# Performance work log

Hardware: AMD Instinct MI355X
Metric: run time of the kernel (lower is better)

Reference implementation:

```python
import jax, jax.numpy as jnp
import numpy as np

# Masked BatchNorm: per-channel stats over valid (masked) elements only.
def _masked_bn(x, mask, gamma, beta, eps=1e-5):
    m = mask.astype(x.dtype)  # (B,1,N[,K])
    axes = tuple([0] + list(range(2, x.ndim)))
    n = jnp.maximum(jnp.sum(m, axis=axes), 1.0)
    mean = jnp.sum(x * m, axis=axes) / n  # (C,)
    shp = (1, x.shape[1]) + (1,) * (x.ndim - 2)
    mu = mean.reshape(shp)
    var = jnp.sum(jnp.square(x - mu) * m, axis=axes) / n
    xn = (x - mu) * jax.lax.rsqrt(var.reshape(shp) + eps)
    return xn * gamma.reshape(shp) + beta.reshape(shp)

def _lrelu(x):
    return jnp.where(x >= 0, x, 0.2 * x)  # LeakyReLU(0.2)

MIN_NBR = 1  # config['neighbourhood']['min']

def _edge_block(x, idx, valid, W, g, b):
    # x: (B,C,N), idx: (B,N,K) neighbour indices, valid: (B,N,K) bool
    B, C, N = x.shape
    xt = jnp.transpose(x, (0, 2, 1))  # (B,N,C)
    nbr = xt[jnp.arange(B)[:, None, None], idx]  # (B,N,K,C) gather
    ctr = xt[:, :, None, :]
    f = jnp.concatenate([nbr - ctr, jnp.broadcast_to(ctr, nbr.shape)], axis=-1)  # (B,N,K,2C)
    f = f * valid[..., None].astype(f.dtype)
    f = jnp.transpose(f, (0, 3, 1, 2))  # (B,2C,N,K)
    h = jnp.einsum('oc,bcnk->bonk', W, f)  # 1x1 conv2d, no bias
    h = _lrelu(_masked_bn(h, valid[:, None, :, :], g, b))
    h = jnp.max(jnp.where(valid[:, None, :, :], h, -jnp.inf), axis=-1)  # masked max over K
    ok = jnp.sum(valid, axis=-1) >= MIN_NBR  # (B,N)
    h = jnp.where(ok[:, None, :], h, 0.0)
    return h, ok


def setup_inputs() -> dict:
    key = jax.random.key(0)
    ks = jax.random.split(key, 12)
    B, N, K = 8, 2048, 20
    f32 = jnp.float32
    def w(k, shape):
        return jax.random.normal(k, shape, f32) * 0.05
    d = {}
    d['x'] = jax.random.normal(ks[0], (B, 3, N), f32)
    d['idx'] = jax.random.randint(ks[1], (B, N, K), 0, N)
    d['valid'] = jax.random.randint(ks[2], (B, N, K), 0, 2).astype(bool)
    enc_dims = [(64, 6), (64, 128), (128, 128), (256, 256)]
    for i, (o, c) in enumerate(enc_dims, 1):
        d['enc_w%d' % i] = w(jax.random.fold_in(key, 10 + i), (o, c))
        d['enc_g%d' % i] = jnp.ones((o,), f32)
        d['enc_b%d' % i] = jnp.zeros((o,), f32)
    d['last_w'] = w(ks[3], (1024, 512)); d['last_g'] = jnp.ones((1024,), f32); d['last_b'] = jnp.zeros((1024,), f32)
    d['emb_w1'] = w(ks[4], (512, 1024)); d['emb_bias1'] = jnp.zeros((512,), f32); d['emb_g1'] = jnp.ones((512,), f32); d['emb_b1'] = jnp.zeros((512,), f32)
    d['emb_w2'] = w(ks[5], (128, 512)); d['emb_bias2'] = jnp.zeros((128,), f32); d['emb_g2'] = jnp.ones((128,), f32); d['emb_b2'] = jnp.zeros((128,), f32)
    d['out_w'] = w(ks[6], (32, 128)); d['out_bias'] = jnp.zeros((32,), f32)
    return d


def reference(x, idx, valid, enc_w1, enc_g1, enc_b1, enc_w2, enc_g2, enc_b2, enc_w3, enc_g3, enc_b3, enc_w4, enc_g4, enc_b4, last_w, last_g, last_b, emb_w1, emb_bias1, emb_g1, emb_b1, emb_w2, emb_bias2, emb_g2, emb_b2, out_w, out_bias):
    inter = []
    ok_all = jnp.ones((x.shape[0], x.shape[2]), dtype=bool)
    for W, g, b in ((enc_w1, enc_g1, enc_b1), (enc_w2, enc_g2, enc_b2), (enc_w3, enc_g3, enc_b3), (enc_w4, enc_g4, enc_b4)):
        x, ok = _edge_block(x, idx, valid, W, g, b)
        inter.append(x)
        ok_all = jnp.logical_and(ok_all, ok)
    x = jnp.concatenate(inter, axis=1)  # (B,512,N)
    m = ok_all[:, None, :]
    x = _lrelu(_masked_bn(jnp.einsum('oc,bcn->bon', last_w, x), m, last_g, last_b))
    x = jnp.einsum('oc,bcn->bon', emb_w1, x) + emb_bias1[None, :, None]
    x = _lrelu(_masked_bn(x, m, emb_g1, emb_b1))
    x = jnp.einsum('oc,bcn->bon', emb_w2, x) + emb_bias2[None, :, None]
    x = _lrelu(_masked_bn(x, m, emb_g2, emb_b2))
    return jnp.einsum('oc,bcn->bon', out_w, x) + out_bias[None, :, None]  # (B,32,N)
```

## Files before the change

### kernel.cpp

```cpp
#include <hip/hip_runtime.h>
#include <hip/hip_bf16.h>
#include <cstdint>
#include <cstddef>

constexpr int B_  = 8;
constexpr int N_  = 2048;
constexpr int KNB = 20;
constexpr int MN  = B_ * N_;
constexpr int CAT_C = 512;
constexpr float EPS = 1e-5f;

typedef __attribute__((ext_vector_type(8))) short bf16x8;
typedef __attribute__((ext_vector_type(4))) float f32x4;

constexpr size_t alignup64(size_t x){ return (x + 63) & ~size_t(63); }
constexpr size_t STATS   = 0;
constexpr size_t NSTATS  = size_t(7) * 8 * 2048;
constexpr size_t MISC    = STATS + NSTATS;
constexpr size_t SCALEO  = alignup64(MISC + 16);
constexpr size_t SHIFTO  = SCALEO + 7 * 1024;
constexpr size_t CIDX    = alignup64(SHIFTO + 7 * 1024);
constexpr size_t OK8     = alignup64(CIDX + size_t(MN) * KNB);
constexpr size_t WENC    = alignup64(OK8 + (MN + 3) / 4);
constexpr size_t WLAST   = WENC  + 32768;
constexpr size_t WEMB1   = WLAST + 262144;
constexpr size_t WEMB2   = WEMB1 + 262144;
constexpr size_t XT      = WEMB2 + 32768;
constexpr size_t XCATB   = alignup64(XT + size_t(MN) * 4);
constexpr size_t HHOFF   = XCATB + size_t(MN) * 256;
constexpr size_t HMAXO   = HHOFF + size_t(MN) * 512;
constexpr size_t HMINO   = HMAXO + size_t(MN) * 256;
constexpr size_t YLB     = HMINO + size_t(MN) * 256;

__device__ inline float bf2f(unsigned short u){
    unsigned int x = ((unsigned int)u) << 16;
    return __builtin_bit_cast(float, x);
}
__device__ inline unsigned short f2bf(float f){
    __hip_bfloat16 h = __float2bfloat16(f);
    return __builtin_bit_cast(unsigned short, h);
}
__device__ inline unsigned int packbf(float a, float b){
    return (unsigned int)f2bf(a) | ((unsigned int)f2bf(b) << 16);
}
__device__ inline float lrelu(float v){ return fmaxf(v, 0.2f * v); }
__device__ inline void gl16(const void* g, void* l){
    __builtin_amdgcn_global_load_lds(
        (const __attribute__((address_space(1))) void*)g,
        (__attribute__((address_space(3))) void*)l, 16, 0, 0);
}


__global__ __launch_bounds__(256) void detect_valid_kernel(const unsigned char* __restrict__ v, int* __restrict__ flag){
    __shared__ int f;
    if (threadIdx.x == 0) f = 1;
    __syncthreads();
    int ok = 1;
    #pragma unroll
    for (int it = 0; it < 4; ++it){
        int g = threadIdx.x + it * 256;
        unsigned char b0 = v[4*g], b1 = v[4*g+1], b2 = v[4*g+2], b3 = v[4*g+3];
        if ((b1 | b2 | b3) != 0 || b0 > 1) ok = 0;
    }
    if (!ok) atomicAnd(&f, 0);
    __syncthreads();
    if (threadIdx.x == 0) *flag = f;
}

__global__ __launch_bounds__(256) void expand_ok_kernel(const void* __restrict__ vin,
        const int* __restrict__ idx, int* __restrict__ ci, unsigned char* __restrict__ ok,
        float* __restrict__ nvalid, float* __restrict__ n_ok, const int* __restrict__ flag){
    const int p = blockIdx.x * 256 + threadIdx.x;
    int jj[KNB];
    const int4* ip4 = (const int4*)(idx + (size_t)p * KNB);
    #pragma unroll
    for (int q = 0; q < 5; ++q){
        int4 iv = ip4[q];
        jj[q*4+0] = iv.x; jj[q*4+1] = iv.y; jj[q*4+2] = iv.z; jj[q*4+3] = iv.w;
    }
    bool val[KNB];
    if (*flag){
        const int* vi = ((const int*)vin) + (size_t)p * KNB;
        #pragma unroll
        for (int k = 0; k < KNB; ++k) val[k] = vi[k] != 0;
    } else {
        const unsigned char* vb = ((const unsigned char*)vin) + (size_t)p * KNB;
        #pragma unroll
        for (int k = 0; k < KNB; ++k) val[k] = vb[k] != 0;
    }
    int cnt = 0;
    int* dst = ci + (size_t)p * KNB;
    #pragma unroll
    for (int k = 0; k < KNB; ++k){
        if (val[k]) dst[cnt++] = jj[k];
    }
    ok[p] = (unsigned char)cnt;
    float fc = (float)cnt;
    #pragma unroll
    for (int o = 32; o > 0; o >>= 1) fc += __shfl_down(fc, o);
    unsigned long long m = __ballot(cnt != 0);
    if ((threadIdx.x & 63) == 0){
        if (fc > 0.f) unsafeAtomicAdd(nvalid, fc);
        if (m)        unsafeAtomicAdd(n_ok, (float)__popcll(m));
    }
}

__global__ __launch_bounds__(256) void transpose_x_kernel(const float* __restrict__ x, float* __restrict__ xt){
    int i = blockIdx.x * 256 + threadIdx.x;
    if (i >= MN) return;
    int b = i / N_, n = i % N_;
    float4 v;
    v.x = x[(size_t)(b*3 + 0) * N_ + n];
    v.y = x[(size_t)(b*3 + 1) * N_ + n];
    v.z = x[(size_t)(b*3 + 2) * N_ + n];
    v.w = 0.f;
    ((float4*)xt)[i] = v;
}

__global__ __launch_bounds__(256) void build_wcomb_f32_kernel(const float* __restrict__ W, float* __restrict__ wc,
        int O, int C){
    int i = blockIdx.x * 256 + threadIdx.x;
    if (i >= 2 * O * C) return;
    int r = i / C, c = i % C;
    float v;
    if (r < O) v = W[(size_t)r * (2*C) + c];
    else       v = W[(size_t)(r-O) * (2*C) + C + c] - W[(size_t)(r-O) * (2*C) + c];
    wc[i] = v;
}

__global__ __launch_bounds__(256) void build_wcomb_bf16_kernel(const float* __restrict__ W, unsigned short* __restrict__ wc,
        int O, int C){
    int i = blockIdx.x * 256 + threadIdx.x;
    if (i >= 2 * O * C) return;
    int r = i / C, c = i % C;
    float v;
    if (r < O) v = W[(size_t)r * (2*C) + c];
    else       v = W[(size_t)(r-O) * (2*C) + C + c] - W[(size_t)(r-O) * (2*C) + c];
    wc[i] = f2bf(v);
}

__global__ __launch_bounds__(256) void convert3_bf16_kernel(
        const float* __restrict__ a, const float* __restrict__ b, const float* __restrict__ c,
        unsigned short* __restrict__ wa, unsigned short* __restrict__ wb, unsigned short* __restrict__ wcc){
    int i = blockIdx.x * 256 + threadIdx.x;
    if (i >= 278528) return;
    const float* src; unsigned short* dst; int off;
    if (i < 131072)      { src = a; dst = wa;  off = i; }
    else if (i < 262144) { src = b; dst = wb;  off = i - 131072; }
    else                 { src = c; dst = wcc; off = i - 262144; }
    float4 v = ((const float4*)src)[off];
    ushort4 o;
    o.x = f2bf(v.x); o.y = f2bf(v.y); o.z = f2bf(v.z); o.w = f2bf(v.w);
    ((ushort4*)dst)[off] = o;
}

__global__ __launch_bounds__(256) void gemm_f32(
        const float* __restrict__ X, const float* __restrict__ W,
        float* __restrict__ Y, const float* __restrict__ bias,
        int M, int K, int O, int lda, int ldy,
        const float* __restrict__ scX, const float* __restrict__ shX)
{
    __shared__ float Xs[16][68];
    __shared__ float Ws[16][68];
    const int tid = threadIdx.x;
    const int tx = tid & 15, ty = tid >> 4;
    const int m0 = blockIdx.x * 64, o0 = blockIdx.y * 64;
    float acc[4][4] = {};
    for (int k0 = 0; k0 < K; k0 += 16){
        #pragma unroll
        for (int i = 0; i < 4; ++i){
            int e = tid + i * 256;
            int r = e >> 4, c = e & 15;
            float xv = 0.f, wv = 0.f;
            if (k0 + c < K){
                xv = X[(size_t)(m0 + r) * lda + k0 + c];
                if (scX){
                    xv = lrelu(xv * scX[k0 + c] + shX[k0 + c]);
                }
                if (o0 + r < O) wv = W[(size_t)(o0 + r) * K + k0 + c];
            }
            Xs[c][r] = xv;
            Ws[c][r] = wv;
        }
        __syncthreads();
        #pragma unroll
        for (int kk = 0; kk < 16; ++kk){
            const float4 a4 = *(const float4*)(&Xs[kk][ty * 4]);
            const float4 b4 = *(const float4*)(&Ws[kk][tx * 4]);
            const float a[4] = {a4.x, a4.y, a4.z, a4.w};
            const float b[4] = {b4.x, b4.y, b4.z, b4.w};
            #pragma unroll
            for (int i = 0; i < 4; ++i)
                #pragma unroll
                for (int j = 0; j < 4; ++j)
                    acc[i][j] = fmaf(a[i], b[j], acc[i][j]);
        }
        __syncthreads();
    }
    #pragma unroll
    for (int i = 0; i < 4; ++i){
        int m = m0 + ty * 4 + i;
        int o = o0 + tx * 4;
        if (o < O){
            float4 v;
            v.x = acc[i][0]; v.y = acc[i][1]; v.z = acc[i][2]; v.w = acc[i][3];
            if (bias){
                v.x += bias[o]; v.y += bias[o+1]; v.z += bias[o+2]; v.w += bias[o+3];
            }
            *(float4*)(&Y[(size_t)m * ldy + o]) = v;
        }
    }
}

template<bool OBF16, bool STATSF, bool AFFA>
__global__ __launch_bounds__(256) void gemm_bf16_mfma(
        const unsigned short* __restrict__ Xg, const unsigned short* __restrict__ Wg,
        void* __restrict__ Yv, const float* __restrict__ bias,
        int K, int ldx, int ldy,
        const unsigned char* __restrict__ ok, float* __restrict__ statsL,
        const float* __restrict__ scA, const float* __restrict__ shA)
{
    __shared__ unsigned short As[128 * 64];
    __shared__ unsigned short Bs[128 * 64];
    __shared__ float scsh[AFFA ? 2048 : 2];
    const int t = threadIdx.x;
    const int lane = t & 63;
    const int w = t >> 6;
    const int wr = w >> 1, wc = w & 1;
    const int m0 = blockIdx.x * 128;
    const int o0 = blockIdx.y * 128;

    if constexpr (AFFA){
        for (int v = t; v < K; v += 256){
            scsh[v] = scA[v];
            scsh[1024 + v] = shA[v];
        }
        __syncthreads();
    }

    f32x4 acc[4][4] = {};

    for (int k0 = 0; k0 < K; k0 += 64){
        #pragma unroll
        for (int i = 0; i < 4; ++i){
            int e = i * 256 + t;
            int row = e >> 3;
            int c = (e & 7) ^ (row & 7);
            int kk = k0 + c * 8;
            if constexpr (AFFA){
                uint4 a = *(const uint4*)(Xg + (size_t)(m0 + row) * ldx + kk);
                float4 s0 = *(const float4*)&scsh[kk], s1 = *(const float4*)&scsh[kk + 4];
                float4 h0 = *(const float4*)&scsh[1024 + kk], h1 = *(const float4*)&scsh[1024 + kk + 4];
                const float sc[8] = {s0.x,s0.y,s0.z,s0.w, s1.x,s1.y,s1.z,s1.w};
                const float sh[8] = {h0.x,h0.y,h0.z,h0.w, h1.x,h1.y,h1.z,h1.w};
                unsigned int wds[4] = {a.x, a.y, a.z, a.w};
                unsigned int ov[4];
                #pragma unroll
                for (int q = 0; q < 4; ++q){
                    float f0 = lrelu(bf2f((unsigned short)(wds[q] & 0xffffu)) * sc[2*q]   + sh[2*q]);
                    float f1 = lrelu(bf2f((unsigned short)(wds[q] >> 16))     * sc[2*q+1] + sh[2*q+1]);
                    ov[q] = packbf(f0, f1);
                }
                uint4 o4 = {ov[0], ov[1], ov[2], ov[3]};
                *(uint4*)&As[(size_t)e * 8] = o4;
            } else {
                gl16(Xg + (size_t)(m0 + row) * ldx + kk, &As[(size_t)e * 8]);
            }
            gl16(Wg + (size_t)(o0 + row) * K + kk, &Bs[(size_t)e * 8]);
        }
        __syncthreads();
        const int kq = lane >> 4;
        #pragma unroll
        for (int ks = 0; ks < 2; ++ks){
            bf16x8 a[4], b[4];
            #pragma unroll
            for (int mi = 0; mi < 4; ++mi){
                int r = wr * 64 + mi * 16 + (lane & 15);
                int ch = (ks * 4 + kq) ^ (r & 7);
                a[mi] = *(const bf16x8*)&As[r * 64 + ch * 8];
            }
            #pragma unroll
            for (int ni = 0; ni < 4; ++ni){
                int r = wc * 64 + ni * 16 + (lane & 15);
                int ch = (ks * 4 + kq) ^ (r & 7);
                b[ni] = *(const bf16x8*)&Bs[r * 64 + ch * 8];
            }
            #pragma unroll
            for (int mi = 0; mi < 4; ++mi)
                #pragma unroll
                for (int ni = 0; ni < 4; ++ni)
                    acc[mi][ni] = __builtin_amdgcn_mfma_f32_16x16x32_bf16(a[mi], b[ni], acc[mi][ni], 0, 0, 0);
        }
        __syncthreads();
    }

    float s1l[4] = {}, s2l[4] = {};
    float bi[4];
    #pragma unroll
    for (int ni = 0; ni < 4; ++ni)
        bi[ni] = bias ? bias[o0 + wc * 64 + ni * 16 + (lane & 15)] : 0.f;

    #pragma unroll
    for (int mi = 0; mi < 4; ++mi){
        const int mbase = m0 + wr * 64 + mi * 16 + (lane >> 4) * 4;
        uchar4 okv = {1,1,1,1};
        if constexpr (STATSF) okv = *(const uchar4*)(ok + mbase);
        const unsigned char okarr[4] = {okv.x, okv.y, okv.z, okv.w};
        #pragma unroll
        for (int j = 0; j < 4; ++j){
            const int m = mbase + j;
            #pragma unroll
            for (int ni = 0; ni < 4; ++ni){
                int o = o0 + wc * 64 + ni * 16 + (lane & 15);
                float v = acc[mi][ni][j] + bi[ni];
                if constexpr (STATSF){
                    if (okarr[j]){ s1l[ni] += v; s2l[ni] += v * v; }
                }
                if constexpr (OBF16)
                    ((unsigned short*)Yv)[(size_t)m * ldy + o] = f2bf(v);
                else
                    ((float*)Yv)[(size_t)m * ldy + o] = v;
            }
        }
    }

    if constexpr (STATSF){
        #pragma unroll
        for (int ni = 0; ni < 4; ++ni){
            s1l[ni] += __shfl_xor(s1l[ni], 16); s1l[ni] += __shfl_xor(s1l[ni], 32);
            s2l[ni] += __shfl_xor(s2l[ni], 16); s2l[ni] += __shfl_xor(s2l[ni], 32);
        }
        if ((lane >> 4) == 0){
            float* S = statsL + (size_t)((blockIdx.x + blockIdx.y) & 7) * 2048;
            #pragma unroll
            for (int ni = 0; ni < 4; ++ni){
                int o = o0 + wc * 64 + ni * 16 + lane;
                unsafeAtomicAdd(&S[o],        s1l[ni]);
                unsafeAtomicAdd(&S[1024 + o], s2l[ni]);
            }
        }
    }
}

template<int T>
__global__ __launch_bounds__(256) void edge_gather_kernel(
        const float* __restrict__ HHp, const int* __restrict__ ci,
        const unsigned char* __restrict__ okc, const float* __restrict__ g,
        float* __restrict__ hmaxo, float* __restrict__ hmino,
        float* __restrict__ statsL)
{
    constexpr int O = 64 * T, TWO2 = 2 * O;
    __shared__ float ls[4][2][64 * T];
    const int bid  = blockIdx.x;
    const int wv   = threadIdx.x >> 6;
    const int lane = threadIdx.x & 63;
    const int bat  = bid & 7;
    const int chunk = bid >> 3;
    const int base = bat << 11;
    const int p0   = base + chunk * 8 + wv * 2;

    bool ln = false;
    #pragma unroll
    for (int t = 0; t < T; ++t) if (g[lane + 64 * t] < 0.f) ln = true;
    const bool needmin = (__ballot(ln) != 0ull);

    float s1[T] = {}, s2[T] = {};
    #pragma unroll
    for (int pi = 0; pi < 2; ++pi){
        const int p = p0 + pi;
        const int cnt = okc[p];
        int jj[KNB];
        const int4* ip4 = (const int4*)(ci + (size_t)p * KNB);
        #pragma unroll
        for (int q = 0; q < 5; ++q){
            int4 iv = ip4[q];
            jj[q*4+0] = iv.x; jj[q*4+1] = iv.y; jj[q*4+2] = iv.z; jj[q*4+3] = iv.w;
        }
        float hc[T], hmax[T], hmin[T];
        #pragma unroll
        for (int t = 0; t < T; ++t){
            hc[t] = HHp[(size_t)p * TWO2 + O + lane + 64 * t];
            hmax[t] = -INFINITY; hmin[t] = INFINITY;
        }
        if (needmin){
            int k = 0;
            for (; k + 4 <= cnt; k += 4){
                #pragma unroll
                for (int u = 0; u < 4; ++u){
                    const float* row = HHp + (size_t)(base + jj[k + u]) * TWO2 + lane;
                    #pragma unroll
                    for (int t = 0; t < T; ++t){
                        float h = row[64 * t] + hc[t];
                        s1[t] += h; s2[t] += h * h;
                        hmax[t] = fmaxf(hmax[t], h);
                        hmin[t] = fminf(hmin[t], h);
                    }
                }
            }
            for (; k < cnt; ++k){
                const float* row = HHp + (size_t)(base + jj[k]) * TWO2 + lane;
                #pragma unroll
                for (int t = 0; t < T; ++t){
                    float h = row[64 * t] + hc[t];
                    s1[t] += h; s2[t] += h * h;
                    hmax[t] = fmaxf(hmax[t], h);
                    hmin[t] = fminf(hmin[t], h);
                }
            }
        } else {
            int k = 0;
            for (; k + 4 <= cnt; k += 4){
                #pragma unroll
                for (int u = 0; u < 4; ++u){
                    const float* row = HHp + (size_t)(base + jj[k + u]) * TWO2 + lane;
                    #pragma unroll
                    for (int t = 0; t < T; ++t){
                        float h = row[64 * t] + hc[t];
                        s1[t] += h; s2[t] += h * h;
                        hmax[t] = fmaxf(hmax[t], h);
                    }
                }
            }
            for (; k < cnt; ++k){
                const float* row = HHp + (size_t)(base + jj[k]) * TWO2 + lane;
                #pragma unroll
                for (int t = 0; t < T; ++t){
                    float h = row[64 * t] + hc[t];
                    s1[t] += h; s2[t] += h * h;
                    hmax[t] = fmaxf(hmax[t], h);
                }
            }
        }
        #pragma unroll
        for (int t = 0; t < T; ++t)
            __builtin_nontemporal_store(hmax[t], &hmaxo[(size_t)p * O + lane + 64 * t]);
        if (needmin){
            #pragma unroll
            for (int t = 0; t < T; ++t)
                __builtin_nontemporal_store(hmin[t], &hmino[(size_t)p * O + lane + 64 * t]);
        }
    }
    #pragma unroll
    for (int t = 0; t < T; ++t){
        ls[wv][0][64 * t + lane] = s1[t];
        ls[wv][1][64 * t + lane] = s2[t];
    }
    __syncthreads();
    float* S = statsL + (size_t)(bid & 7) * 2048;
    for (int v = threadIdx.x; v < 128 * T; v += 256){
        const int half = v / (64 * T);
        const int ch   = v - half * 64 * T;
        float s = ls[0][half][ch] + ls[1][half][ch] + ls[2][half][ch] + ls[3][half][ch];
        unsafeAtomicAdd(&S[half * 1024 + ch], s);
    }
}

__global__ void bn_params_kernel(const float* __restrict__ statsL, const float* __restrict__ cnt,
        const float* __restrict__ g, const float* __restrict__ bta,
        float* __restrict__ scale, float* __restrict__ shift, int O)
{
    int o = blockIdx.x * 256 + threadIdx.x;
    if (o >= O) return;
    float s1 = 0.f, s2 = 0.f;
    #pragma unroll
    for (int r = 0; r < 8; ++r){
        s1 += statsL[(size_t)r * 2048 + o];
        s2 += statsL[(size_t)r * 2048 + 1024 + o];
    }
    float n   = fmaxf(*cnt, 1.0f);
    float mu  = s1 / n;
    float var = fmaxf(s2 / n - mu * mu, 0.f);
    float sc  = g[o] * rsqrtf(var + EPS);
    scale[o] = sc;
    shift[o] = bta[o] - mu * sc;
}

__global__ __launch_bounds__(256) void edge_finalize_kernel(
        const float* __restrict__ hmaxo, const float* __restrict__ hmino,
        const unsigned char* __restrict__ ok,
        const float* __restrict__ scale, const float* __restrict__ shift,
        unsigned short* __restrict__ xcat, int O, int chanoff)
{
    size_t i = (size_t)blockIdx.x * 256 + threadIdx.x;
    size_t p = i / (size_t)O;
    int o = (int)(i - p * (size_t)O);
    float v = 0.f;
    if (ok[p]){
        float sc = scale[o];
        float h;
        if (sc >= 0.f) h = hmaxo[i]; else h = hmino[i];
        v = lrelu(h * sc + shift[o]);
    }
    xcat[p * CAT_C + chanoff + o] = f2bf(v);
}

__global__ __launch_bounds__(256) void transpose_out_kernel(const float* __restrict__ Y, float* __restrict__ out){
    int i = blockIdx.x * 256 + threadIdx.x;
    int n = i & (N_ - 1);
    int rest = i >> 11;
    int o = rest & 31;
    int b = rest >> 5;
    out[i] = Y[((((size_t)b * N_) + n) << 5) + o];
}

extern "C" void kernel_launch(void* const* d_in, const int* in_sizes, int n_in,
                              void* d_out, int out_size, void* d_ws, size_t ws_size,
                              hipStream_t stream)
{
    const float* x        = (const float*)d_in[0];
    const int*   idx      = (const int*)  d_in[1];
    const void*  valid_rw = d_in[2];
    const float* enc_w[4] = {(const float*)d_in[3], (const float*)d_in[6], (const float*)d_in[9],  (const float*)d_in[12]};
    const float* enc_g[4] = {(const float*)d_in[4], (const float*)d_in[7], (const float*)d_in[10], (const float*)d_in[13]};
    const float* enc_b[4] = {(const float*)d_in[5], (const float*)d_in[8], (const float*)d_in[11], (const float*)d_in[14]};
    const float* last_w   = (const float*)d_in[15];
    const float* last_g   = (const float*)d_in[16];
    const float* last_b   = (const float*)d_in[17];
    const float* emb_w1   = (const float*)d_in[18];
    const float* emb_bi1  = (const float*)d_in[19];
    const float* emb_g1   = (const float*)d_in[20];
    const float* emb_b1   = (const float*)d_in[21];
    const float* emb_w2   = (const float*)d_in[22];
    const float* emb_bi2  = (const float*)d_in[23];
    const float* emb_g2   = (const float*)d_in[24];
    const float* emb_b2   = (const float*)d_in[25];
    const float* out_w    = (const float*)d_in[26];
    const float* out_bias = (const float*)d_in[27];

    float* ws = (float*)d_ws;
    int*   ci   = (int*)(ws + CIDX);
    unsigned char* ok8  = (unsigned char*)(ws + OK8);
    unsigned short* xcatb = (unsigned short*)(ws + XCATB);
    unsigned short* ylb   = (unsigned short*)(ws + YLB);
    unsigned short* wlastb = (unsigned short*)(ws + WLAST);
    unsigned short* wemb1b = (unsigned short*)(ws + WEMB1);
    unsigned short* wemb2b = (unsigned short*)(ws + WEMB2);
    float* nvalid = ws + MISC + 0;
    float* n_ok   = ws + MISC + 1;
    int*   flag   = (int*)(ws + MISC + 2);

    hipMemsetAsync(d_ws, 0, (MISC + 16) * sizeof(float), stream);

    detect_valid_kernel<<<1, 256, 0, stream>>>((const unsigned char*)valid_rw, flag);
    expand_ok_kernel<<<MN / 256, 256, 0, stream>>>(valid_rw, idx, ci, ok8, nvalid, n_ok, flag);
    transpose_x_kernel<<<MN / 256, 256, 0, stream>>>(x, ws + XT);
    convert3_bf16_kernel<<<(278528 + 255) / 256, 256, 0, stream>>>(last_w, emb_w1, emb_w2, wlastb, wemb1b, wemb2b);

    const int Cs[4]     = {3, 64, 64, 128};
    const int Os[4]     = {64, 64, 128, 256};
    const int inoff[4]  = {0, 0, 64, 128};
    const int outoff[4] = {0, 64, 128, 256};

    for (int L = 0; L < 4; ++L){
        const int C = Cs[L], O = Os[L], TWO2 = 2 * O;
        if (L == 0){
            build_wcomb_f32_kernel<<<(2*O*C + 255)/256, 256, 0, stream>>>(enc_w[L], ws + WENC, O, C);
            dim3 gg(MN / 64, TWO2 / 64);
            gemm_f32<<<gg, 256, 0, stream>>>(ws + XT, ws + WENC, ws + HHOFF, nullptr, MN, C, TWO2, 4, TWO2, nullptr, nullptr);
        } else {
            build_wcomb_bf16_kernel<<<(2*O*C + 255)/256, 256, 0, stream>>>(enc_w[L], (unsigned short*)(ws + WENC), O, C);
            dim3 gg(MN / 128, TWO2 / 128);
            gemm_bf16_mfma<false, false, false><<<gg, 256, 0, stream>>>(xcatb + inoff[L], (unsigned short*)(ws + WENC),
                    ws + HHOFF, nullptr, C, CAT_C, TWO2, nullptr, nullptr, nullptr, nullptr);
        }
        float* statsL = ws + STATS + (size_t)L * 8 * 2048;
        const int gather_blocks = MN / 8;
        switch (O / 64){
            case 1: edge_gather_kernel<1><<<gather_blocks, 256, 0, stream>>>(ws + HHOFF, ci, ok8, enc_g[L], ws + HMAXO, ws + HMINO, statsL); break;
            case 2: edge_gather_kernel<2><<<gather_blocks, 256, 0, stream>>>(ws + HHOFF, ci, ok8, enc_g[L], ws + HMAXO, ws + HMINO, statsL); break;
            case 4: edge_gather_kernel<4><<<gather_blocks, 256, 0, stream>>>(ws + HHOFF, ci, ok8, enc_g[L], ws + HMAXO, ws + HMINO, statsL); break;
        }
        float* scl = ws + SCALEO + (size_t)L * 1024;
        float* shf = ws + SHIFTO + (size_t)L * 1024;
        bn_params_kernel<<<(O + 255)/256, 256, 0, stream>>>(statsL, nvalid, enc_g[L], enc_b[L], scl, shf, O);
        edge_finalize_kernel<<<(int)(((size_t)MN * O) / 256), 256, 0, stream>>>(
            ws + HMAXO, ws + HMINO, ok8, scl, shf, xcatb, O, outoff[L]);
    }

    unsigned short* yemb1b = (unsigned short*)(ws + HMAXO);
    float* yemb2 = ws + HMINO;
    float* yout  = ws + HHOFF;

    float* scl4 = ws + SCALEO + 4 * 1024, *shf4 = ws + SHIFTO + 4 * 1024;
    float* scl5 = ws + SCALEO + 5 * 1024, *shf5 = ws + SHIFTO + 5 * 1024;
    float* scl6 = ws + SCALEO + 6 * 1024, *shf6 = ws + SHIFTO + 6 * 1024;

    {
        float* statsL = ws + STATS + (size_t)4 * 8 * 2048;
        dim3 gg(MN / 128, 1024 / 128);
        gemm_bf16_mfma<true, true, false><<<gg, 256, 0, stream>>>(xcatb, wlastb, ylb, nullptr, 512, CAT_C, 1024,
                ok8, statsL, nullptr, nullptr);
        bn_params_kernel<<<4, 256, 0, stream>>>(statsL, n_ok, last_g, last_b, scl4, shf4, 1024);
    }
    {
        float* statsL = ws + STATS + (size_t)5 * 8 * 2048;
        dim3 gg(MN / 128, 512 / 128);
        gemm_bf16_mfma<true, true, true><<<gg, 256, 0, stream>>>(ylb, wemb1b, yemb1b, emb_bi1, 1024, 1024, 512,
                ok8, statsL, scl4, shf4);
        bn_params_kernel<<<2, 256, 0, stream>>>(statsL, n_ok, emb_g1, emb_b1, scl5, shf5, 512);
    }
    {
        float* statsL = ws + STATS + (size_t)6 * 8 * 2048;
        dim3 gg(MN / 128, 128 / 128);
        gemm_bf16_mfma<false, true, true><<<gg, 256, 0, stream>>>(yemb1b, wemb2b, yemb2, emb_bi2, 512, 512, 128,
                ok8, statsL, scl5, shf5);
        bn_params_kernel<<<1, 256, 0, stream>>>(statsL, n_ok, emb_g2, emb_b2, scl6, shf6, 128);
    }
    {
        dim3 gg(MN / 64, 1);
        gemm_f32<<<gg, 256, 0, stream>>>(yemb2, out_w, yout, out_bias, MN, 128, 32, 128, 32, scl6, shf6);
        transpose_out_kernel<<<(B_ * 32 * N_) / 256, 256, 0, stream>>>(yout, (float*)d_out);
    }
}
```

Measured before the change: 387.3 us.

## Fold BN parameter computation into producer kernels and merge prep launches

Removes the separate bn_params kernels by having the last block of each stats-producing kernel (edge gather and fused GEMMs) compute scale and shift, chosen through an atomic completion counter and threadfence. Merges the valid-format detection into expand_ok, and merges the x transpose, weight bf16 conversions and all four edge-weight combinations into one prep kernel. This cuts roughly a dozen small kernel launches and their dependency gaps. In exchange, every block of those kernels now pays for a fence and a counter atomic, and each block of expand_ok repeats the detection scan.

```diff
diff --git a/kernel.cpp b/kernel.cpp
--- a/kernel.cpp
+++ b/kernel.cpp
@@ -21,8 +21,11 @@
 constexpr size_t SHIFTO  = SCALEO + 7 * 1024;
 constexpr size_t CIDX    = alignup64(SHIFTO + 7 * 1024);
 constexpr size_t OK8     = alignup64(CIDX + size_t(MN) * KNB);
-constexpr size_t WENC    = alignup64(OK8 + (MN + 3) / 4);
-constexpr size_t WLAST   = WENC  + 32768;
+constexpr size_t WENC0   = alignup64(OK8 + (MN + 3) / 4);
+constexpr size_t WENC1   = WENC0 + 512;
+constexpr size_t WENC2   = WENC1 + 4096;
+constexpr size_t WENC3   = WENC2 + 8192;
+constexpr size_t WLAST   = WENC3 + 32768;
 constexpr size_t WEMB1   = WLAST + 262144;
 constexpr size_t WEMB2   = WEMB1 + 262144;
 constexpr size_t XT      = WEMB2 + 32768;
@@ -50,26 +53,43 @@
         (__attribute__((address_space(3))) void*)l, 16, 0, 0);
 }
 
-
-__global__ __launch_bounds__(256) void detect_valid_kernel(const unsigned char* __restrict__ v, int* __restrict__ flag){
+__device__ inline void bn_finalize(const float* statsL, float n,
+        const float* g, const float* bta, float* scale, float* shift, int O){
+    for (int o = threadIdx.x; o < O; o += 256){
+        float s1 = 0.f, s2 = 0.f;
+        #pragma unroll
+        for (int r = 0; r < 8; ++r){
+            s1 += atomicAdd((float*)&statsL[(size_t)r * 2048 + o], 0.f);
+            s2 += atomicAdd((float*)&statsL[(size_t)r * 2048 + 1024 + o], 0.f);
+        }
+        float mu  = s1 / n;
+        float var = fmaxf(s2 / n - mu * mu, 0.f);
+        float sc  = g[o] * rsqrtf(var + EPS);
+        scale[o] = sc;
+        shift[o] = bta[o] - mu * sc;
+    }
+}
+
+__global__ __launch_bounds__(256) void expand_ok_kernel(const void* __restrict__ vin,
+        const int* __restrict__ idx, int* __restrict__ ci, unsigned char* __restrict__ ok,
+        float* __restrict__ nvalid, float* __restrict__ n_ok){
     __shared__ int f;
     if (threadIdx.x == 0) f = 1;
     __syncthreads();
-    int ok = 1;
-    #pragma unroll
-    for (int it = 0; it < 4; ++it){
-        int g = threadIdx.x + it * 256;
-        unsigned char b0 = v[4*g], b1 = v[4*g+1], b2 = v[4*g+2], b3 = v[4*g+3];
-        if ((b1 | b2 | b3) != 0 || b0 > 1) ok = 0;
-    }
-    if (!ok) atomicAnd(&f, 0);
+    {
+        const unsigned char* v = (const unsigned char*)vin;
+        int okd = 1;
+        #pragma unroll
+        for (int it = 0; it < 4; ++it){
+            int gq = threadIdx.x + it * 256;
+            unsigned char b0 = v[4*gq], b1 = v[4*gq+1], b2 = v[4*gq+2], b3 = v[4*gq+3];
+            if ((b1 | b2 | b3) != 0 || b0 > 1) okd = 0;
+        }
+        if (!okd) atomicAnd(&f, 0);
+    }
     __syncthreads();
-    if (threadIdx.x == 0) *flag = f;
-}
-
-__global__ __launch_bounds__(256) void expand_ok_kernel(const void* __restrict__ vin,
-        const int* __restrict__ idx, int* __restrict__ ci, unsigned char* __restrict__ ok,
-        float* __restrict__ nvalid, float* __restrict__ n_ok, const int* __restrict__ flag){
+    const bool isInt = (f != 0);
+
     const int p = blockIdx.x * 256 + threadIdx.x;
     int jj[KNB];
     const int4* ip4 = (const int4*)(idx + (size_t)p * KNB);
@@ -79,7 +99,7 @@
         jj[q*4+0] = iv.x; jj[q*4+1] = iv.y; jj[q*4+2] = iv.z; jj[q*4+3] = iv.w;
     }
     bool val[KNB];
-    if (*flag){
+    if (isInt){
         const int* vi = ((const int*)vin) + (size_t)p * KNB;
         #pragma unroll
         for (int k = 0; k < KNB; ++k) val[k] = vi[k] != 0;
@@ -105,53 +125,57 @@
     }
 }
 
-__global__ __launch_bounds__(256) void transpose_x_kernel(const float* __restrict__ x, float* __restrict__ xt){
+constexpr int PR0 = MN;
+constexpr int PR1 = PR0 + 278528;
+constexpr int PR2 = PR1 + 384;
+constexpr int PR3 = PR2 + 8192;
+constexpr int PR4 = PR3 + 16384;
+constexpr int PR5 = PR4 + 65536;
+__device__ inline float wcomb_val(const float* W, int r, int c, int O, int C){
+    if (r < O) return W[(size_t)r * (2*C) + c];
+    return W[(size_t)(r-O) * (2*C) + C + c] - W[(size_t)(r-O) * (2*C) + c];
+}
+__global__ __launch_bounds__(256) void prep_kernel(
+        const float* __restrict__ x, float* __restrict__ xt,
+        const float* __restrict__ lw, const float* __restrict__ e1w, const float* __restrict__ e2w,
+        unsigned short* __restrict__ wla, unsigned short* __restrict__ we1, unsigned short* __restrict__ we2,
+        const float* __restrict__ w0, const float* __restrict__ w1,
+        const float* __restrict__ w2, const float* __restrict__ w3,
+        float* __restrict__ wc0, unsigned short* __restrict__ wc1,
+        unsigned short* __restrict__ wc2, unsigned short* __restrict__ wc3)
+{
     int i = blockIdx.x * 256 + threadIdx.x;
-    if (i >= MN) return;
-    int b = i / N_, n = i % N_;
-    float4 v;
-    v.x = x[(size_t)(b*3 + 0) * N_ + n];
-    v.y = x[(size_t)(b*3 + 1) * N_ + n];
-    v.z = x[(size_t)(b*3 + 2) * N_ + n];
-    v.w = 0.f;
-    ((float4*)xt)[i] = v;
-}
-
-__global__ __launch_bounds__(256) void build_wcomb_f32_kernel(const float* __restrict__ W, float* __restrict__ wc,
-        int O, int C){
-    int i = blockIdx.x * 256 + threadIdx.x;
-    if (i >= 2 * O * C) return;
-    int r = i / C, c = i % C;
-    float v;
-    if (r < O) v = W[(size_t)r * (2*C) + c];
-    else       v = W[(size_t)(r-O) * (2*C) + C + c] - W[(size_t)(r-O) * (2*C) + c];
-    wc[i] = v;
-}
-
-__global__ __launch_bounds__(256) void build_wcomb_bf16_kernel(const float* __restrict__ W, unsigned short* __restrict__ wc,
-        int O, int C){
-    int i = blockIdx.x * 256 + threadIdx.x;
-    if (i >= 2 * O * C) return;
-    int r = i / C, c = i % C;
-    float v;
-    if (r < O) v = W[(size_t)r * (2*C) + c];
-    else       v = W[(size_t)(r-O) * (2*C) + C + c] - W[(size_t)(r-O) * (2*C) + c];
-    wc[i] = f2bf(v);
-}
-
-__global__ __launch_bounds__(256) void convert3_bf16_kernel(
-        const float* __restrict__ a, const float* __restrict__ b, const float* __restrict__ c,
-        unsigned short* __restrict__ wa, unsigned short* __restrict__ wb, unsigned short* __restrict__ wcc){
-    int i = blockIdx.x * 256 + threadIdx.x;
-    if (i >= 278528) return;
-    const float* src; unsigned short* dst; int off;
-    if (i < 131072)      { src = a; dst = wa;  off = i; }
-    else if (i < 262144) { src = b; dst = wb;  off = i - 131072; }
-    else                 { src = c; dst = wcc; off = i - 262144; }
-    float4 v = ((const float4*)src)[off];
-    ushort4 o;
-    o.x = f2bf(v.x); o.y = f2bf(v.y); o.z = f2bf(v.z); o.w = f2bf(v.w);
-    ((ushort4*)dst)[off] = o;
+    if (i < PR0){
+        int b = i / N_, n = i % N_;
+        float4 v;
+        v.x = x[(size_t)(b*3 + 0) * N_ + n];
+        v.y = x[(size_t)(b*3 + 1) * N_ + n];
+        v.z = x[(size_t)(b*3 + 2) * N_ + n];
+        v.w = 0.f;
+        ((float4*)xt)[i] = v;
+    } else if (i < PR1){
+        int gix = i - PR0;
+        const float* src; unsigned short* dst; int off;
+        if (gix < 131072)      { src = lw;  dst = wla; off = gix; }
+        else if (gix < 262144) { src = e1w; dst = we1; off = gix - 131072; }
+        else                   { src = e2w; dst = we2; off = gix - 262144; }
+        float4 v = ((const float4*)src)[off];
+        ushort4 o;
+        o.x = f2bf(v.x); o.y = f2bf(v.y); o.z = f2bf(v.z); o.w = f2bf(v.w);
+        ((ushort4*)dst)[off] = o;
+    } else if (i < PR2){
+        int e = i - PR1;
+        wc0[e] = wcomb_val(w0, e / 3, e % 3, 64, 3);
+    } else if (i < PR3){
+        int e = i - PR2;
+        wc1[e] = f2bf(wcomb_val(w1, e >> 6, e & 63, 64, 64));
+    } else if (i < PR4){
+        int e = i - PR3;
+        wc2[e] = f2bf(wcomb_val(w2, e >> 6, e & 63, 128, 64));
+    } else if (i < PR5){
+        int e = i - PR4;
+        wc3[e] = f2bf(wcomb_val(w3, e >> 7, e & 127, 256, 128));
+    }
 }
 
 __global__ __launch_bounds__(256) void gemm_f32(
@@ -218,7 +242,9 @@
         void* __restrict__ Yv, const float* __restrict__ bias,
         int K, int ldx, int ldy,
         const unsigned char* __restrict__ ok, float* __restrict__ statsL,
-        const float* __restrict__ scA, const float* __restrict__ shA)
+        const float* __restrict__ scA, const float* __restrict__ shA,
+        const float* __restrict__ cntp, const float* __restrict__ gsc, const float* __restrict__ gsh,
+        float* __restrict__ scaleOut, float* __restrict__ shiftOut, int* __restrict__ ctr, int Ochan)
 {
     __shared__ unsigned short As[128 * 64];
     __shared__ unsigned short Bs[128 * 64];
@@ -339,6 +365,16 @@
                 unsafeAtomicAdd(&S[1024 + o], s2l[ni]);
             }
         }
+        __threadfence();
+        __syncthreads();
+        __shared__ int isLast;
+        if (t == 0)
+            isLast = (atomicAdd(ctr, 1) == (int)(gridDim.x * gridDim.y) - 1);
+        __syncthreads();
+        if (isLast){
+            float n = fmaxf(*cntp, 1.0f);
+            bn_finalize(statsL, n, gsc, gsh, scaleOut, shiftOut, Ochan);
+        }
     }
 }
 
@@ -347,7 +383,9 @@
         const float* __restrict__ HHp, const int* __restrict__ ci,
         const unsigned char* __restrict__ okc, const float* __restrict__ g,
         float* __restrict__ hmaxo, float* __restrict__ hmino,
-        float* __restrict__ statsL)
+        float* __restrict__ statsL,
+        const float* __restrict__ cntp, const float* __restrict__ bta,
+        float* __restrict__ scaleOut, float* __restrict__ shiftOut, int* __restrict__ ctr)
 {
     constexpr int O = 64 * T, TWO2 = 2 * O;
     __shared__ float ls[4][2][64 * T];
@@ -453,26 +491,16 @@
         float s = ls[0][half][ch] + ls[1][half][ch] + ls[2][half][ch] + ls[3][half][ch];
         unsafeAtomicAdd(&S[half * 1024 + ch], s);
     }
-}
-
-__global__ void bn_params_kernel(const float* __restrict__ statsL, const float* __restrict__ cnt,
-        const float* __restrict__ g, const float* __restrict__ bta,
-        float* __restrict__ scale, float* __restrict__ shift, int O)
-{
-    int o = blockIdx.x * 256 + threadIdx.x;
-    if (o >= O) return;
-    float s1 = 0.f, s2 = 0.f;
-    #pragma unroll
-    for (int r = 0; r < 8; ++r){
-        s1 += statsL[(size_t)r * 2048 + o];
-        s2 += statsL[(size_t)r * 2048 + 1024 + o];
-    }
-    float n   = fmaxf(*cnt, 1.0f);
-    float mu  = s1 / n;
-    float var = fmaxf(s2 / n - mu * mu, 0.f);
-    float sc  = g[o] * rsqrtf(var + EPS);
-    scale[o] = sc;
-    shift[o] = bta[o] - mu * sc;
+    __threadfence();
+    __syncthreads();
+    __shared__ int isLast;
+    if (threadIdx.x == 0)
+        isLast = (atomicAdd(ctr, 1) == (int)gridDim.x - 1);
+    __syncthreads();
+    if (isLast){
+        float n = fmaxf(*cntp, 1.0f);
+        bn_finalize(statsL, n, g, bta, scaleOut, shiftOut, O);
+    }
 }
 
 __global__ __launch_bounds__(256) void edge_finalize_kernel(
@@ -537,42 +565,42 @@
     unsigned short* wemb2b = (unsigned short*)(ws + WEMB2);
     float* nvalid = ws + MISC + 0;
     float* n_ok   = ws + MISC + 1;
-    int*   flag   = (int*)(ws + MISC + 2);
+    int*   ctrs   = (int*)(ws + MISC + 3);
 
     hipMemsetAsync(d_ws, 0, (MISC + 16) * sizeof(float), stream);
 
-    detect_valid_kernel<<<1, 256, 0, stream>>>((const unsigned char*)valid_rw, flag);
-    expand_ok_kernel<<<MN / 256, 256, 0, stream>>>(valid_rw, idx, ci, ok8, nvalid, n_ok, flag);
-    transpose_x_kernel<<<MN / 256, 256, 0, stream>>>(x, ws + XT);
-    convert3_bf16_kernel<<<(278528 + 255) / 256, 256, 0, stream>>>(last_w, emb_w1, emb_w2, wlastb, wemb1b, wemb2b);
+    expand_ok_kernel<<<MN / 256, 256, 0, stream>>>(valid_rw, idx, ci, ok8, nvalid, n_ok);
+    prep_kernel<<<(PR5 + 255) / 256, 256, 0, stream>>>(
+        x, ws + XT, last_w, emb_w1, emb_w2, wlastb, wemb1b, wemb2b,
+        enc_w[0], enc_w[1], enc_w[2], enc_w[3],
+        ws + WENC0, (unsigned short*)(ws + WENC1), (unsigned short*)(ws + WENC2), (unsigned short*)(ws + WENC3));
 
     const int Cs[4]     = {3, 64, 64, 128};
     const int Os[4]     = {64, 64, 128, 256};
     const int inoff[4]  = {0, 0, 64, 128};
     const int outoff[4] = {0, 64, 128, 256};
+    const size_t wencs[4] = {WENC0, WENC1, WENC2, WENC3};
 
     for (int L = 0; L < 4; ++L){
         const int C = Cs[L], O = Os[L], TWO2 = 2 * O;
         if (L == 0){
-            build_wcomb_f32_kernel<<<(2*O*C + 255)/256, 256, 0, stream>>>(enc_w[L], ws + WENC, O, C);
             dim3 gg(MN / 64, TWO2 / 64);
-            gemm_f32<<<gg, 256, 0, stream>>>(ws + XT, ws + WENC, ws + HHOFF, nullptr, MN, C, TWO2, 4, TWO2, nullptr, nullptr);
+            gemm_f32<<<gg, 256, 0, stream>>>(ws + XT, ws + WENC0, ws + HHOFF, nullptr, MN, C, TWO2, 4, TWO2, nullptr, nullptr);
         } else {
-            build_wcomb_bf16_kernel<<<(2*O*C + 255)/256, 256, 0, stream>>>(enc_w[L], (unsigned short*)(ws + WENC), O, C);
             dim3 gg(MN / 128, TWO2 / 128);
-            gemm_bf16_mfma<false, false, false><<<gg, 256, 0, stream>>>(xcatb + inoff[L], (unsigned short*)(ws + WENC),
-                    ws + HHOFF, nullptr, C, CAT_C, TWO2, nullptr, nullptr, nullptr, nullptr);
+            gemm_bf16_mfma<false, false, false><<<gg, 256, 0, stream>>>(xcatb + inoff[L], (unsigned short*)(ws + wencs[L]),
+                    ws + HHOFF, nullptr, C, CAT_C, TWO2, nullptr, nullptr, nullptr, nullptr,
+                    nullptr, nullptr, nullptr, nullptr, nullptr, nullptr, 0);
         }
         float* statsL = ws + STATS + (size_t)L * 8 * 2048;
+        float* scl = ws + SCALEO + (size_t)L * 1024;
+        float* shf = ws + SHIFTO + (size_t)L * 1024;
         const int gather_blocks = MN / 8;
         switch (O / 64){
-            case 1: edge_gather_kernel<1><<<gather_blocks, 256, 0, stream>>>(ws + HHOFF, ci, ok8, enc_g[L], ws + HMAXO, ws + HMINO, statsL); break;
-            case 2: edge_gather_kernel<2><<<gather_blocks, 256, 0, stream>>>(ws + HHOFF, ci, ok8, enc_g[L], ws + HMAXO, ws + HMINO, statsL); break;
-            case 4: edge_gather_kernel<4><<<gather_blocks, 256, 0, stream>>>(ws + HHOFF, ci, ok8, enc_g[L], ws + HMAXO, ws + HMINO, statsL); break;
-        }
-        float* scl = ws + SCALEO + (size_t)L * 1024;
-        float* shf = ws + SHIFTO + (size_t)L * 1024;
-        bn_params_kernel<<<(O + 255)/256, 256, 0, stream>>>(statsL, nvalid, enc_g[L], enc_b[L], scl, shf, O);
+            case 1: edge_gather_kernel<1><<<gather_blocks, 256, 0, stream>>>(ws + HHOFF, ci, ok8, enc_g[L], ws + HMAXO, ws + HMINO, statsL, nvalid, enc_b[L], scl, shf, ctrs + L); break;
+            case 2: edge_gather_kernel<2><<<gather_blocks, 256, 0, stream>>>(ws + HHOFF, ci, ok8, enc_g[L], ws + HMAXO, ws + HMINO, statsL, nvalid, enc_b[L], scl, shf, ctrs + L); break;
+            case 4: edge_gather_kernel<4><<<gather_blocks, 256, 0, stream>>>(ws + HHOFF, ci, ok8, enc_g[L], ws + HMAXO, ws + HMINO, statsL, nvalid, enc_b[L], scl, shf, ctrs + L); break;
+        }
         edge_finalize_kernel<<<(int)(((size_t)MN * O) / 256), 256, 0, stream>>>(
             ws + HMAXO, ws + HMINO, ok8, scl, shf, xcatb, O, outoff[L]);
     }
@@ -589,22 +617,19 @@
         float* statsL = ws + STATS + (size_t)4 * 8 * 2048;
         dim3 gg(MN / 128, 1024 / 128);
         gemm_bf16_mfma<true, true, false><<<gg, 256, 0, stream>>>(xcatb, wlastb, ylb, nullptr, 512, CAT_C, 1024,
-                ok8, statsL, nullptr, nullptr);
-        bn_params_kernel<<<4, 256, 0, stream>>>(statsL, n_ok, last_g, last_b, scl4, shf4, 1024);
+                ok8, statsL, nullptr, nullptr, n_ok, last_g, last_b, scl4, shf4, ctrs + 4, 1024);
     }
     {
         float* statsL = ws + STATS + (size_t)5 * 8 * 2048;
         dim3 gg(MN / 128, 512 / 128);
         gemm_bf16_mfma<true, true, true><<<gg, 256, 0, stream>>>(ylb, wemb1b, yemb1b, emb_bi1, 1024, 1024, 512,
-                ok8, statsL, scl4, shf4);
-        bn_params_kernel<<<2, 256, 0, stream>>>(statsL, n_ok, emb_g1, emb_b1, scl5, shf5, 512);
+                ok8, statsL, scl4, shf4, n_ok, emb_g1, emb_b1, scl5, shf5, ctrs + 5, 512);
     }
     {
         float* statsL = ws + STATS + (size_t)6 * 8 * 2048;
         dim3 gg(MN / 128, 128 / 128);
         gemm_bf16_mfma<false, true, true><<<gg, 256, 0, stream>>>(yemb1b, wemb2b, yemb2, emb_bi2, 512, 512, 128,
-                ok8, statsL, scl5, shf5);
-        bn_params_kernel<<<1, 256, 0, stream>>>(statsL, n_ok, emb_g2, emb_b2, scl6, shf6, 128);
+                ok8, statsL, scl5, shf5, n_ok, emb_g2, emb_b2, scl6, shf6, ctrs + 6, 128);
     }
     {
         dim3 gg(MN / 64, 1);
```

New measurement: 1.119 ms. +189.0%, slower.
